# Optimization experiments

Hardware: AMD Instinct MI355X
Metric: run time of the kernel (lower is better)

## Reference

```python
import jax, jax.numpy as jnp
import numpy as np

N, K, G, E, OUT = 50000, 32, 512, 400000, 8
EPS = 1e-8


def setup_inputs() -> dict:
    key = jax.random.key(0)
    ks = jax.random.split(key, 9)
    X = jax.random.uniform(ks[0], (N, G), dtype=jnp.float32)          # counts-like, non-negative
    Mu = jax.random.uniform(ks[1], (K, G), dtype=jnp.float32)
    Var = jax.random.uniform(ks[2], (K, G), dtype=jnp.float32) + 0.5  # keep variances bounded away from 0
    edge_index = jax.random.randint(ks[3], (2, E), 0, N)
    # learned parameters
    W = jax.random.normal(ks[4], (N, K), dtype=jnp.float32) * 0.1     # module inits zeros; small randn for non-trivial grads
    S = jnp.ones((N, 1), jnp.float32)
    glorot = float(np.sqrt(6.0 / (G + OUT)))
    Wl = jax.random.uniform(ks[5], (G, OUT), jnp.float32, -glorot, glorot)
    bl = jnp.zeros((OUT,), jnp.float32)
    Wr = jax.random.uniform(ks[6], (G, OUT), jnp.float32, -glorot, glorot)
    br = jnp.zeros((OUT,), jnp.float32)
    att = jax.random.normal(ks[7], (OUT,), jnp.float32) * 0.3
    return dict(X=X, Mu=Mu, Var=Var, W=W, S=S, Wl=Wl, bl=bl, Wr=Wr, br=br, att=att, edge_index=edge_index)


def reference(X, Mu, Var, W, S, Wl, bl, Wr, br, att, edge_index):
    P = jax.nn.softmax(W, axis=1)                                     # [N,K]

    # Gaussian NLL term: F[n,k] = -0.5 * sum_g (X[n,g] - Mu[k,g]*S[n])^2 / Var[k,g]
    # expanded into three GEMM-shaped contractions to avoid the [N,K,G] intermediate
    inv_var = 1.0 / Var                                               # [K,G]
    q1 = (X * X) @ inv_var.T                                          # [N,K]
    q2 = X @ (Mu * inv_var).T                                         # [N,K]
    q3 = jnp.sum(Mu * Mu * inv_var, axis=1)                           # [K]
    s = S[:, 0]                                                       # [N]
    Fmat = -0.5 * (q1 - 2.0 * s[:, None] * q2 + (s * s)[:, None] * q3[None, :])
    ll_prot = jnp.sum(P * Fmat) / X.shape[0]

    # GATv2 attention (heads=1, out=8, no self loops): only alpha is consumed downstream
    src, dst = edge_index[0], edge_index[1]
    xl = X @ Wl + bl                                                  # source transform [N,8]
    xr = X @ Wr + br                                                  # target transform [N,8]
    e = jax.nn.leaky_relu(xl[src] + xr[dst], 0.2) @ att               # [E]
    # segment softmax over edges grouped by destination node
    m = jax.lax.stop_gradient(jax.ops.segment_max(e, dst, num_segments=N))
    ex = jnp.exp(e - m[dst])
    denom = jax.ops.segment_sum(ex, dst, num_segments=N)
    alpha = ex / denom[dst]                                           # [E]

    ce_space = -jnp.sum(P[src] * alpha[:, None] * jnp.log(P[dst] + EPS)) / X.shape[0]
    return ll_prot, ce_space, P
```

## Files before the change

kernel.cpp:

```cpp
#include <hip/hip_runtime.h>
#include <hip/hip_bf16.h>
#include <math.h>

#define N_NODES 50000
#define K_COMP  32
#define G_DIM   512
#define E_EDGES 400000
#define OUT_DIM 8
#define EPSV    1e-8f

#define NPB 32
#define NB_NODE ((N_NODES + NPB - 1) / NPB)
#define NB_E1   ((E_EDGES + 255) / 256)
#define NB_CE   ((E_EDGES / 2 + 255) / 256)

typedef __attribute__((ext_vector_type(8))) short short8;
typedef __attribute__((ext_vector_type(8))) unsigned short ushort8;
typedef __attribute__((ext_vector_type(4))) unsigned short ushort4v;
typedef __attribute__((ext_vector_type(4))) float f32x4;

static const size_t OFF_T    = 0;
static const size_t OFF_Q3   = OFF_T + 80 * 512;
static const size_t OFF_SRC  = OFF_Q3 + 64;
static const size_t OFF_DST  = OFF_SRC + (size_t)N_NODES * 32;
static const size_t OFF_CON  = OFF_DST + (size_t)N_NODES * 32;
static const size_t OFF_DEN  = OFF_CON + E_EDGES;
static const size_t OFF_PLL  = OFF_DEN + N_NODES;
static const size_t OFF_PCE  = OFF_PLL + 8192;

__device__ __forceinline__ unsigned short f2bf(float f) {
    __hip_bfloat16 h = __float2bfloat16(f);
    return *(unsigned short*)&h;
}
__device__ __forceinline__ float bf2f(unsigned short u) {
    unsigned v = ((unsigned)u) << 16;
    return __uint_as_float(v);
}

__global__ __launch_bounds__(256)
void prep_kernel(const float* __restrict__ Var, const float* __restrict__ Mu,
                 const float* __restrict__ Wl, const float* __restrict__ Wr,
                 unsigned short* __restrict__ Tb, float* __restrict__ den,
                 float* __restrict__ q3) {
    int idx = blockIdx.x * 256 + threadIdx.x;
    if (idx < 80 * 512) {
        int r = idx >> 9;
        int g = idx & 511;
        float v;
        if (r < 32)      v = 1.0f / Var[r * 512 + g];
        else if (r < 64) { int k = r - 32; v = Mu[k * 512 + g] / Var[k * 512 + g]; }
        else if (r < 72) { int o = r - 64; v = Wl[g * 8 + o]; }
        else             { int o = r - 72; v = Wr[g * 8 + o]; }
        int dest = ((g >> 5) * 5 + (r >> 4)) * 512 + (r & 15) * 32 + (((g & 31) >> 3) << 3) + (g & 7);
        Tb[dest] = f2bf(v);
    }
    if (idx < N_NODES) den[idx] = 0.0f;

    if (blockIdx.x < 32) {
        int k = blockIdx.x;
        int t = threadIdx.x;
        float s = 0.0f;
        for (int g = t; g < 512; g += 256) {
            float mu = Mu[k * 512 + g];
            s += mu * mu / Var[k * 512 + g];
        }
        for (int off = 32; off; off >>= 1) s += __shfl_down(s, off);
        __shared__ float sQ[4];
        if ((t & 63) == 0) sQ[t >> 6] = s;
        __syncthreads();
        if (t == 0) q3[k] = sQ[0] + sQ[1] + sQ[2] + sQ[3];
    }
}

__global__ __launch_bounds__(256, 4)
void node_kernel(const float* __restrict__ X, const float* __restrict__ W,
                 const float* __restrict__ S, const float* __restrict__ bl,
                 const float* __restrict__ br, const unsigned short* __restrict__ Tb,
                 const float* __restrict__ q3, float* __restrict__ outP,
                 float* __restrict__ srcRec, float* __restrict__ dstRec,
                 float* __restrict__ pll) {
    __shared__ float sAccH[4][NPB][80];

    const int t = threadIdx.x;
    const int lane = t & 63;
    const int wq = t >> 6;
    const int col = lane & 15;
    const int kg  = lane >> 4;

    const int n0 = blockIdx.x * NPB;
    int nodeA = n0 + col;
    int nodeB = n0 + 16 + col;
    if (nodeA >= N_NODES) nodeA = N_NODES - 1;
    if (nodeB >= N_NODES) nodeB = N_NODES - 1;
    const float* xrowA = X + (size_t)nodeA * 512 + wq * 128 + kg * 8;
    const float* xrowB = X + (size_t)nodeB * 512 + wq * 128 + kg * 8;

    f32x4 accA[5], accB[5];
#pragma unroll
    for (int i = 0; i < 5; ++i) {
        accA[i] = (f32x4){0.f, 0.f, 0.f, 0.f};
        accB[i] = (f32x4){0.f, 0.f, 0.f, 0.f};
    }

#pragma unroll
    for (int it = 0; it < 4; ++it) {
        const unsigned short* bbase =
            Tb + (size_t)(wq * 4 + it) * 5 * 512 + col * 32 + kg * 8;
        short8 b0 = *(const short8*)(bbase);
        short8 b1 = *(const short8*)(bbase + 512);
        short8 b2 = *(const short8*)(bbase + 1024);
        short8 b3 = *(const short8*)(bbase + 1536);
        short8 b4 = *(const short8*)(bbase + 2048);

        float4 va0 = *(const float4*)(xrowA + it * 32);
        float4 va1 = *(const float4*)(xrowA + it * 32 + 4);
        float4 vb0 = *(const float4*)(xrowB + it * 32);
        float4 vb1 = *(const float4*)(xrowB + it * 32 + 4);

        short8 axA, axA2, axB, axB2;
        axA[0] = (short)f2bf(va0.x); axA[1] = (short)f2bf(va0.y);
        axA[2] = (short)f2bf(va0.z); axA[3] = (short)f2bf(va0.w);
        axA[4] = (short)f2bf(va1.x); axA[5] = (short)f2bf(va1.y);
        axA[6] = (short)f2bf(va1.z); axA[7] = (short)f2bf(va1.w);
        axA2[0] = (short)f2bf(va0.x * va0.x); axA2[1] = (short)f2bf(va0.y * va0.y);
        axA2[2] = (short)f2bf(va0.z * va0.z); axA2[3] = (short)f2bf(va0.w * va0.w);
        axA2[4] = (short)f2bf(va1.x * va1.x); axA2[5] = (short)f2bf(va1.y * va1.y);
        axA2[6] = (short)f2bf(va1.z * va1.z); axA2[7] = (short)f2bf(va1.w * va1.w);
        axB[0] = (short)f2bf(vb0.x); axB[1] = (short)f2bf(vb0.y);
        axB[2] = (short)f2bf(vb0.z); axB[3] = (short)f2bf(vb0.w);
        axB[4] = (short)f2bf(vb1.x); axB[5] = (short)f2bf(vb1.y);
        axB[6] = (short)f2bf(vb1.z); axB[7] = (short)f2bf(vb1.w);
        axB2[0] = (short)f2bf(vb0.x * vb0.x); axB2[1] = (short)f2bf(vb0.y * vb0.y);
        axB2[2] = (short)f2bf(vb0.z * vb0.z); axB2[3] = (short)f2bf(vb0.w * vb0.w);
        axB2[4] = (short)f2bf(vb1.x * vb1.x); axB2[5] = (short)f2bf(vb1.y * vb1.y);
        axB2[6] = (short)f2bf(vb1.z * vb1.z); axB2[7] = (short)f2bf(vb1.w * vb1.w);

        accA[0] = __builtin_amdgcn_mfma_f32_16x16x32_bf16(axA2, b0, accA[0], 0, 0, 0);
        accB[0] = __builtin_amdgcn_mfma_f32_16x16x32_bf16(axB2, b0, accB[0], 0, 0, 0);
        accA[1] = __builtin_amdgcn_mfma_f32_16x16x32_bf16(axA2, b1, accA[1], 0, 0, 0);
        accB[1] = __builtin_amdgcn_mfma_f32_16x16x32_bf16(axB2, b1, accB[1], 0, 0, 0);
        accA[2] = __builtin_amdgcn_mfma_f32_16x16x32_bf16(axA,  b2, accA[2], 0, 0, 0);
        accB[2] = __builtin_amdgcn_mfma_f32_16x16x32_bf16(axB,  b2, accB[2], 0, 0, 0);
        accA[3] = __builtin_amdgcn_mfma_f32_16x16x32_bf16(axA,  b3, accA[3], 0, 0, 0);
        accB[3] = __builtin_amdgcn_mfma_f32_16x16x32_bf16(axB,  b3, accB[3], 0, 0, 0);
        accA[4] = __builtin_amdgcn_mfma_f32_16x16x32_bf16(axA,  b4, accA[4], 0, 0, 0);
        accB[4] = __builtin_amdgcn_mfma_f32_16x16x32_bf16(axB,  b4, accB[4], 0, 0, 0);
    }

#pragma unroll
    for (int ot = 0; ot < 5; ++ot)
#pragma unroll
        for (int r = 0; r < 4; ++r) {
            sAccH[wq][kg * 4 + r][ot * 16 + col]      = accA[ot][r];
            sAccH[wq][16 + kg * 4 + r][ot * 16 + col] = accB[ot][r];
        }
    __syncthreads();

    const int nn = t >> 3;
    const int j = t & 7;
    const int n = n0 + nn;
    const bool valid = n < N_NODES;
    const int nc = valid ? n : N_NODES - 1;

    float sv = S[nc];
    float sv2 = sv * sv;
    float4 wv4 = *(const float4*)(W + (size_t)nc * 32 + j * 4);
    float w[4] = {wv4.x, wv4.y, wv4.z, wv4.w};
    float wm = fmaxf(fmaxf(w[0], w[1]), fmaxf(w[2], w[3]));
    wm = fmaxf(wm, __shfl_xor(wm, 1));
    wm = fmaxf(wm, __shfl_xor(wm, 2));
    wm = fmaxf(wm, __shfl_xor(wm, 4));
    float p[4], ps = 0.0f;
#pragma unroll
    for (int i = 0; i < 4; ++i) { p[i] = __expf(w[i] - wm); ps += p[i]; }
    ps += __shfl_xor(ps, 1);
    ps += __shfl_xor(ps, 2);
    ps += __shfl_xor(ps, 4);
    float inv = 1.0f / ps;

    float pv[4];
    ushort4v pb, lb;
    float ll = 0.0f;
#pragma unroll
    for (int i = 0; i < 4; ++i) {
        int k = j * 4 + i;
        float P_ = p[i] * inv;
        pv[i] = P_;
        pb[i] = f2bf(P_);
        lb[i] = f2bf(__logf(P_ + EPSV));
        float q1k = sAccH[0][nn][k] + sAccH[1][nn][k] +
                    sAccH[2][nn][k] + sAccH[3][nn][k];
        float q2k = sAccH[0][nn][32 + k] + sAccH[1][nn][32 + k] +
                    sAccH[2][nn][32 + k] + sAccH[3][nn][32 + k];
        float f = -0.5f * (q1k - 2.0f * sv * q2k + sv2 * q3[k]);
        ll = fmaf(P_, f, ll);
    }
    ll += __shfl_xor(ll, 1);
    ll += __shfl_xor(ll, 2);
    ll += __shfl_xor(ll, 4);
    float llacc = (j == 0 && valid) ? ll : 0.0f;

    if (valid) {
        size_t base = (size_t)n * 32 + j * 4;
        float2* op = (float2*)(outP + base);
        op[0] = make_float2(pv[0], pv[1]);
        op[1] = make_float2(pv[2], pv[3]);

        float* sr = srcRec + (size_t)n * 32;
        float* dr = dstRec + (size_t)n * 32;
        *(ushort4v*)&((unsigned short*)sr)[16 + j * 4] = pb;
        *(ushort4v*)&((unsigned short*)dr)[16 + j * 4] = lb;
        sr[j] = (sAccH[0][nn][64 + j] + sAccH[1][nn][64 + j] +
                 sAccH[2][nn][64 + j] + sAccH[3][nn][64 + j]) + bl[j];
        dr[j] = (sAccH[0][nn][72 + j] + sAccH[1][nn][72 + j] +
                 sAccH[2][nn][72 + j] + sAccH[3][nn][72 + j]) + br[j];
    }

    for (int off = 32; off; off >>= 1) llacc += __shfl_down(llacc, off);
    if (lane == 0) pll[blockIdx.x * 4 + wq] = llacc;
}

__global__ __launch_bounds__(256, 4)
void edge1_kernel(const int* __restrict__ ei, const float* __restrict__ srcRec,
                  const float* __restrict__ dstRec, const float* __restrict__ att,
                  float* __restrict__ contrib, float* __restrict__ den) {
    int i = blockIdx.x * 256 + threadIdx.x;
    if (i >= E_EDGES) return;
    int s = ei[i];
    int d = ei[E_EDGES + i];
    const float4* sp = (const float4*)(srcRec + (size_t)s * 32);
    const float4* dp = (const float4*)(dstRec + (size_t)d * 32);
    float4 a0 = sp[0], a1 = sp[1];
    float4 b0 = dp[0], b1 = dp[1];
    const ushort8* pp = (const ushort8*)(sp + 2);
    const ushort8* lp = (const ushort8*)(dp + 2);
    ushort8 pa = pp[0], pb_ = pp[1], pc = pp[2], pd = pp[3];
    ushort8 la = lp[0], lb_ = lp[1], lc = lp[2], ld = lp[3];
    const float4* atp = (const float4*)att;
    float4 t0 = atp[0], t1 = atp[1];
    float at[8] = {t0.x, t0.y, t0.z, t0.w, t1.x, t1.y, t1.z, t1.w};
    float h[8] = {a0.x + b0.x, a0.y + b0.y, a0.z + b0.z, a0.w + b0.w,
                  a1.x + b1.x, a1.y + b1.y, a1.z + b1.z, a1.w + b1.w};
    float ev = 0.0f;
#pragma unroll
    for (int q = 0; q < 8; ++q) {
        float hv = h[q];
        hv = hv > 0.0f ? hv : 0.2f * hv;
        ev = fmaf(hv, at[q], ev);
    }
    float x = __expf(ev);
    atomicAdd(den + d, x);

    float dot = 0.0f;
#pragma unroll
    for (int r = 0; r < 8; ++r) {
        dot = fmaf(bf2f(pa[r]),  bf2f(la[r]),  dot);
        dot = fmaf(bf2f(pb_[r]), bf2f(lb_[r]), dot);
        dot = fmaf(bf2f(pc[r]),  bf2f(lc[r]),  dot);
        dot = fmaf(bf2f(pd[r]),  bf2f(ld[r]),  dot);
    }
    contrib[i] = x * dot;
}

__global__ __launch_bounds__(256, 4)
void edge2_kernel(const int* __restrict__ ei, const float* __restrict__ contrib,
                  const float* __restrict__ den, float* __restrict__ pce) {
    const int t = threadIdx.x;
    const int base = (blockIdx.x * 256 + t) * 2;
    float ce = 0.0f;
    if (base < E_EDGES) {
        int2 dd = *(const int2*)&ei[E_EDGES + base];
        float2 cv = *(const float2*)&contrib[base];
        ce = cv.x / den[dd.x] + cv.y / den[dd.y];
    }
    for (int off = 32; off; off >>= 1) ce += __shfl_down(ce, off);
    __shared__ float sC[4];
    if ((t & 63) == 0) sC[t >> 6] = ce;
    __syncthreads();
    if (t == 0) pce[blockIdx.x] = sC[0] + sC[1] + sC[2] + sC[3];
}

__global__ __launch_bounds__(256)
void finalize_kernel(const float* __restrict__ pll, const float* __restrict__ pce,
                     float* __restrict__ out) {
    const int t = threadIdx.x;
    float a = 0.0f, b = 0.0f;
    for (int i = t; i < NB_NODE * 4; i += 256) a += pll[i];
    for (int i = t; i < NB_CE; i += 256) b += pce[i];
    for (int off = 32; off; off >>= 1) {
        a += __shfl_down(a, off);
        b += __shfl_down(b, off);
    }
    __shared__ float sA[4], sB[4];
    if ((t & 63) == 0) { sA[t >> 6] = a; sB[t >> 6] = b; }
    __syncthreads();
    if (t == 0) {
        float ll = sA[0] + sA[1] + sA[2] + sA[3];
        float ce = sB[0] + sB[1] + sB[2] + sB[3];
        out[0] = ll / (float)N_NODES;
        out[1] = -ce / (float)N_NODES;
    }
}

extern "C" void kernel_launch(void* const* d_in, const int* in_sizes, int n_in,
                              void* d_out, int out_size, void* d_ws, size_t ws_size,
                              hipStream_t stream) {
    const float* X   = (const float*)d_in[0];
    const float* Mu  = (const float*)d_in[1];
    const float* Var = (const float*)d_in[2];
    const float* W   = (const float*)d_in[3];
    const float* S   = (const float*)d_in[4];
    const float* Wl  = (const float*)d_in[5];
    const float* bl  = (const float*)d_in[6];
    const float* Wr  = (const float*)d_in[7];
    const float* br  = (const float*)d_in[8];
    const float* att = (const float*)d_in[9];
    const int*   ei  = (const int*)d_in[10];
    float* out = (float*)d_out;
    float* ws  = (float*)d_ws;

    unsigned short* Tb     = (unsigned short*)(ws + OFF_T);
    float*          q3     = ws + OFF_Q3;
    float*          srcRec = ws + OFF_SRC;
    float*          dstRec = ws + OFF_DST;
    float*          contrib= ws + OFF_CON;
    float*          den    = ws + OFF_DEN;
    float*          pll    = ws + OFF_PLL;
    float*          pce    = ws + OFF_PCE;

    prep_kernel<<<(N_NODES + 255) / 256, 256, 0, stream>>>(Var, Mu, Wl, Wr, Tb, den, q3);
    node_kernel<<<NB_NODE, 256, 0, stream>>>(X, W, S, bl, br, Tb, q3,
                                             out + 2, srcRec, dstRec, pll);
    edge1_kernel<<<NB_E1, 256, 0, stream>>>(ei, srcRec, dstRec, att, contrib, den);
    edge2_kernel<<<NB_CE, 256, 0, stream>>>(ei, contrib, den, pce);
    finalize_kernel<<<1, 256, 0, stream>>>(pll, pce, out);
}
```

Before: 77.02 us.

## Split each edge across two lanes and fold finalize into edge2 via ticket

The edge kernel now assigns two threads per edge, one gathering the source record and one the destination record, and exchanges the halves with lane shuffles to compute the attention logit and the bf16 dot product. This spreads the 128-byte random gathers over more lanes to raise memory-level parallelism. The separate finalize launch is removed: edge2 uses a global atomic ticket so the last block performs the final reduction, saving one kernel launch at the cost of a fence and an atomic per block.

```diff
diff --git a/kernel.cpp b/kernel.cpp
--- a/kernel.cpp
+++ b/kernel.cpp
@@ -11,7 +11,7 @@
 
 #define NPB 32
 #define NB_NODE ((N_NODES + NPB - 1) / NPB)
-#define NB_E1   ((E_EDGES + 255) / 256)
+#define NB_E1   (E_EDGES / 128)
 #define NB_CE   ((E_EDGES / 2 + 255) / 256)
 
 typedef __attribute__((ext_vector_type(8))) short short8;
@@ -27,6 +27,7 @@
 static const size_t OFF_DEN  = OFF_CON + E_EDGES;
 static const size_t OFF_PLL  = OFF_DEN + N_NODES;
 static const size_t OFF_PCE  = OFF_PLL + 8192;
+static const size_t OFF_TK   = OFF_PCE + 1024;
 
 __device__ __forceinline__ unsigned short f2bf(float f) {
     __hip_bfloat16 h = __float2bfloat16(f);
@@ -35,13 +36,19 @@
 __device__ __forceinline__ float bf2f(unsigned short u) {
     unsigned v = ((unsigned)u) << 16;
     return __uint_as_float(v);
+}
+__device__ __forceinline__ float bf2f_lo(unsigned u) {
+    return __uint_as_float(u << 16);
+}
+__device__ __forceinline__ float bf2f_hi(unsigned u) {
+    return __uint_as_float(u & 0xffff0000u);
 }
 
 __global__ __launch_bounds__(256)
 void prep_kernel(const float* __restrict__ Var, const float* __restrict__ Mu,
                  const float* __restrict__ Wl, const float* __restrict__ Wr,
                  unsigned short* __restrict__ Tb, float* __restrict__ den,
-                 float* __restrict__ q3) {
+                 float* __restrict__ q3, unsigned* __restrict__ ticket) {
     int idx = blockIdx.x * 256 + threadIdx.x;
     if (idx < 80 * 512) {
         int r = idx >> 9;
@@ -55,6 +62,7 @@
         Tb[dest] = f2bf(v);
     }
     if (idx < N_NODES) den[idx] = 0.0f;
+    if (idx == 0) *ticket = 0u;
 
     if (blockIdx.x < 32) {
         int k = blockIdx.x;
@@ -224,47 +232,84 @@
 void edge1_kernel(const int* __restrict__ ei, const float* __restrict__ srcRec,
                   const float* __restrict__ dstRec, const float* __restrict__ att,
                   float* __restrict__ contrib, float* __restrict__ den) {
-    int i = blockIdx.x * 256 + threadIdx.x;
-    if (i >= E_EDGES) return;
-    int s = ei[i];
-    int d = ei[E_EDGES + i];
-    const float4* sp = (const float4*)(srcRec + (size_t)s * 32);
-    const float4* dp = (const float4*)(dstRec + (size_t)d * 32);
-    float4 a0 = sp[0], a1 = sp[1];
-    float4 b0 = dp[0], b1 = dp[1];
-    const ushort8* pp = (const ushort8*)(sp + 2);
-    const ushort8* lp = (const ushort8*)(dp + 2);
-    ushort8 pa = pp[0], pb_ = pp[1], pc = pp[2], pd = pp[3];
-    ushort8 la = lp[0], lb_ = lp[1], lc = lp[2], ld = lp[3];
+    const int t = threadIdx.x;
+    const int e = blockIdx.x * 128 + (t >> 1);
+    const int side = t & 1;
+
+    const int idx = ei[side * E_EDGES + e];
+    const float* rec = (side ? dstRec : srcRec) + (size_t)idx * 32;
+    const float4* rp = (const float4*)rec;
+    float4 x0 = rp[0];
+    float4 x1 = rp[1];
+    const uint4* qp = (const uint4*)rec;
+    uint4 qa = qp[2];
+    uint4 qb = qp[3];
+    uint4 qc = qp[4];
+    uint4 qd = qp[5];
+
     const float4* atp = (const float4*)att;
-    float4 t0 = atp[0], t1 = atp[1];
-    float at[8] = {t0.x, t0.y, t0.z, t0.w, t1.x, t1.y, t1.z, t1.w};
-    float h[8] = {a0.x + b0.x, a0.y + b0.y, a0.z + b0.z, a0.w + b0.w,
-                  a1.x + b1.x, a1.y + b1.y, a1.z + b1.z, a1.w + b1.w};
-    float ev = 0.0f;
-#pragma unroll
-    for (int q = 0; q < 8; ++q) {
-        float hv = h[q];
-        hv = hv > 0.0f ? hv : 0.2f * hv;
-        ev = fmaf(hv, at[q], ev);
-    }
+    float4 at0 = atp[0], at1 = atp[1];
+
+    float4 sx = side ? x0 : x1;
+    float4 rx;
+    rx.x = __shfl_xor(sx.x, 1);
+    rx.y = __shfl_xor(sx.y, 1);
+    rx.z = __shfl_xor(sx.z, 1);
+    rx.w = __shfl_xor(sx.w, 1);
+    float4 hx = side ? make_float4(rx.x + x1.x, rx.y + x1.y, rx.z + x1.z, rx.w + x1.w)
+                     : make_float4(x0.x + rx.x, x0.y + rx.y, x0.z + rx.z, x0.w + rx.w);
+    float4 av = side ? at1 : at0;
+    float evp = 0.0f;
+    {
+        float h0 = hx.x > 0.f ? hx.x : 0.2f * hx.x;
+        float h1 = hx.y > 0.f ? hx.y : 0.2f * hx.y;
+        float h2 = hx.z > 0.f ? hx.z : 0.2f * hx.z;
+        float h3 = hx.w > 0.f ? hx.w : 0.2f * hx.w;
+        evp = fmaf(h0, av.x, fmaf(h1, av.y, fmaf(h2, av.z, h3 * av.w)));
+    }
+    float ev = evp + __shfl_xor(evp, 1);
     float x = __expf(ev);
-    atomicAdd(den + d, x);
-
-    float dot = 0.0f;
-#pragma unroll
-    for (int r = 0; r < 8; ++r) {
-        dot = fmaf(bf2f(pa[r]),  bf2f(la[r]),  dot);
-        dot = fmaf(bf2f(pb_[r]), bf2f(lb_[r]), dot);
-        dot = fmaf(bf2f(pc[r]),  bf2f(lc[r]),  dot);
-        dot = fmaf(bf2f(pd[r]),  bf2f(ld[r]),  dot);
-    }
-    contrib[i] = x * dot;
-}
-
-__global__ __launch_bounds__(256, 4)
-void edge2_kernel(const int* __restrict__ ei, const float* __restrict__ contrib,
-                  const float* __restrict__ den, float* __restrict__ pce) {
+
+    unsigned s0 = side ? qa.x : qc.x, s1 = side ? qa.y : qc.y;
+    unsigned s2 = side ? qa.z : qc.z, s3 = side ? qa.w : qc.w;
+    unsigned s4 = side ? qb.x : qd.x, s5 = side ? qb.y : qd.y;
+    unsigned s6 = side ? qb.z : qd.z, s7 = side ? qb.w : qd.w;
+    unsigned r0 = __shfl_xor(s0, 1), r1 = __shfl_xor(s1, 1);
+    unsigned r2 = __shfl_xor(s2, 1), r3 = __shfl_xor(s3, 1);
+    unsigned r4 = __shfl_xor(s4, 1), r5 = __shfl_xor(s5, 1);
+    unsigned r6 = __shfl_xor(s6, 1), r7 = __shfl_xor(s7, 1);
+    unsigned o0 = side ? qc.x : qa.x, o1 = side ? qc.y : qa.y;
+    unsigned o2 = side ? qc.z : qa.z, o3 = side ? qc.w : qa.w;
+    unsigned o4 = side ? qd.x : qb.x, o5 = side ? qd.y : qb.y;
+    unsigned o6 = side ? qd.z : qb.z, o7 = side ? qd.w : qb.w;
+    float dotp = 0.0f;
+    dotp = fmaf(bf2f_lo(o0), bf2f_lo(r0), dotp);
+    dotp = fmaf(bf2f_hi(o0), bf2f_hi(r0), dotp);
+    dotp = fmaf(bf2f_lo(o1), bf2f_lo(r1), dotp);
+    dotp = fmaf(bf2f_hi(o1), bf2f_hi(r1), dotp);
+    dotp = fmaf(bf2f_lo(o2), bf2f_lo(r2), dotp);
+    dotp = fmaf(bf2f_hi(o2), bf2f_hi(r2), dotp);
+    dotp = fmaf(bf2f_lo(o3), bf2f_lo(r3), dotp);
+    dotp = fmaf(bf2f_hi(o3), bf2f_hi(r3), dotp);
+    dotp = fmaf(bf2f_lo(o4), bf2f_lo(r4), dotp);
+    dotp = fmaf(bf2f_hi(o4), bf2f_hi(r4), dotp);
+    dotp = fmaf(bf2f_lo(o5), bf2f_lo(r5), dotp);
+    dotp = fmaf(bf2f_hi(o5), bf2f_hi(r5), dotp);
+    dotp = fmaf(bf2f_lo(o6), bf2f_lo(r6), dotp);
+    dotp = fmaf(bf2f_hi(o6), bf2f_hi(r6), dotp);
+    dotp = fmaf(bf2f_lo(o7), bf2f_lo(r7), dotp);
+    dotp = fmaf(bf2f_hi(o7), bf2f_hi(r7), dotp);
+    float dot = dotp + __shfl_xor(dotp, 1);
+
+    if (side) atomicAdd(den + idx, x);
+    else      contrib[e] = x * dot;
+}
+
+__global__ __launch_bounds__(256)
+void edge2_final_kernel(const int* __restrict__ ei, const float* __restrict__ contrib,
+                        const float* __restrict__ den, const float* __restrict__ pll,
+                        float* __restrict__ pce, unsigned* __restrict__ ticket,
+                        float* __restrict__ out) {
     const int t = threadIdx.x;
     const int base = (blockIdx.x * 256 + t) * 2;
     float ce = 0.0f;
@@ -275,15 +320,19 @@
     }
     for (int off = 32; off; off >>= 1) ce += __shfl_down(ce, off);
     __shared__ float sC[4];
+    __shared__ int lastFlag;
     if ((t & 63) == 0) sC[t >> 6] = ce;
     __syncthreads();
-    if (t == 0) pce[blockIdx.x] = sC[0] + sC[1] + sC[2] + sC[3];
-}
-
-__global__ __launch_bounds__(256)
-void finalize_kernel(const float* __restrict__ pll, const float* __restrict__ pce,
-                     float* __restrict__ out) {
-    const int t = threadIdx.x;
+    if (t == 0) {
+        pce[blockIdx.x] = sC[0] + sC[1] + sC[2] + sC[3];
+        __threadfence();
+        unsigned old = atomicAdd(ticket, 1u);
+        lastFlag = (old == NB_CE - 1);
+    }
+    __syncthreads();
+    if (!lastFlag) return;
+    __threadfence();
+
     float a = 0.0f, b = 0.0f;
     for (int i = t; i < NB_NODE * 4; i += 256) a += pll[i];
     for (int i = t; i < NB_CE; i += 256) b += pce[i];
@@ -296,9 +345,9 @@
     __syncthreads();
     if (t == 0) {
         float ll = sA[0] + sA[1] + sA[2] + sA[3];
-        float ce = sB[0] + sB[1] + sB[2] + sB[3];
+        float cesum = sB[0] + sB[1] + sB[2] + sB[3];
         out[0] = ll / (float)N_NODES;
-        out[1] = -ce / (float)N_NODES;
+        out[1] = -cesum / (float)N_NODES;
     }
 }
 
@@ -327,11 +376,11 @@
     float*          den    = ws + OFF_DEN;
     float*          pll    = ws + OFF_PLL;
     float*          pce    = ws + OFF_PCE;
-
-    prep_kernel<<<(N_NODES + 255) / 256, 256, 0, stream>>>(Var, Mu, Wl, Wr, Tb, den, q3);
+    unsigned*       ticket = (unsigned*)(ws + OFF_TK);
+
+    prep_kernel<<<(N_NODES + 255) / 256, 256, 0, stream>>>(Var, Mu, Wl, Wr, Tb, den, q3, ticket);
     node_kernel<<<NB_NODE, 256, 0, stream>>>(X, W, S, bl, br, Tb, q3,
                                              out + 2, srcRec, dstRec, pll);
     edge1_kernel<<<NB_E1, 256, 0, stream>>>(ei, srcRec, dstRec, att, contrib, den);
-    edge2_kernel<<<NB_CE, 256, 0, stream>>>(ei, contrib, den, pce);
-    finalize_kernel<<<1, 256, 0, stream>>>(pll, pce, out);
-}
+    edge2_final_kernel<<<NB_CE, 256, 0, stream>>>(ei, contrib, den, pll, pce, ticket, out);
+}
```

Result: slower. 89.86 us (+16.7%).
